# Kernel optimization log

Measured on AMD Instinct MI355X. Metric: run time of the kernel, lower is better.

Reference implementation:

```python
import jax, jax.numpy as jnp
import numpy as np

TWO_PI = 2.0 * np.pi
B, S_IN, S_OUT, K, HID = 1024, 4096, 4096, 8, 512
EPS = 1e-6


def setup_inputs() -> dict:
    key = jax.random.key(0)
    k1, k2, k3, k4, k5, k6, k7, k8 = jax.random.split(key, 8)
    x_in = jax.random.uniform(k1, (B, S_OUT), dtype=jnp.float32) * TWO_PI
    x_passive = jax.random.normal(k2, (B, S_IN), dtype=jnp.float32)
    log_density = jax.random.normal(k3, (B, 1), dtype=jnp.float32)
    # MLP params (nn.Linear default-ish init scale)
    lim1 = 1.0 / np.sqrt(S_IN)
    lim2 = 1.0 / np.sqrt(HID)
    w1 = jax.random.uniform(k4, (S_IN, HID), jnp.float32, -lim1, lim1)
    b1 = jax.random.uniform(k5, (HID,), jnp.float32, -lim1, lim1)
    w2 = jax.random.uniform(k6, (HID, S_OUT * 3 * K), jnp.float32, -lim2, lim2)
    b2 = jax.random.uniform(k7, (S_OUT * 3 * K,), jnp.float32, -lim2, lim2)
    phase_shift = jax.random.uniform(k8, (1,), jnp.float32)
    return {"x_in": x_in, "x_passive": x_passive, "log_density": log_density,
            "w1": w1, "b1": b1, "w2": w2, "b2": b2, "phase_shift": phase_shift}


def reference(x_in, x_passive, log_density, w1, b1, w2, b2, phase_shift):
    # normalise network input with global mean / (unbiased) std, as torch does
    xn = (x_passive - x_passive.mean()) / x_passive.std(ddof=1)
    # dense network: Linear -> tanh -> Linear -> tanh (final_activation=activation)
    net = jnp.tanh(jnp.tanh(xn @ w1 + b1) @ w2 + b2)            # (B, S*3K)
    net = net.reshape(-1, S_OUT, 3 * K)
    h_raw, w_raw, d_raw = net[..., :K], net[..., K:2 * K], net[..., 2 * K:]
    h_norm = jax.nn.softmax(h_raw, axis=2) * TWO_PI              # (B,S,K)
    w_norm = jax.nn.softmax(w_raw, axis=2) * TWO_PI
    d_norm = jax.nn.softplus(d_raw)
    bshape = (h_norm.shape[0], S_OUT, 1)
    x_kp = jnp.concatenate([jnp.full(bshape, -EPS, h_norm.dtype),
                            jnp.cumsum(w_norm, axis=2)], axis=2)  # (B,S,K+1)
    phi_kp = jnp.concatenate([jnp.zeros(bshape, h_norm.dtype),
                              jnp.cumsum(h_norm, axis=2)], axis=2)
    x = x_in[..., None]                                          # (B,S,1)
    # searchsorted (left) per element: count of knots strictly less than x, minus 1
    k_ind = jnp.sum(x_kp < x, axis=2, keepdims=True) - 1         # (B,S,1) int
    k_ind = jnp.clip(k_ind, 0, K - 1)
    g = lambda a, i: jnp.take_along_axis(a, i, axis=2)
    w_k = g(w_norm, k_ind)
    h_k = g(h_norm, k_ind)
    s_k = h_k / w_k
    d_k = g(d_norm, k_ind)
    d_kp1 = g(d_norm, (k_ind + 1) % K)
    x_km1 = g(x_kp, k_ind)
    phi_km1 = g(phi_kp, k_ind)
    alpha = (x - x_km1) / w_k
    a1m = alpha * (1.0 - alpha)
    denom = s_k + (d_kp1 + d_k - 2.0 * s_k) * a1m
    phi_out = (phi_km1 + h_k * (s_k * alpha ** 2 + d_k * a1m) / denom)[..., 0]
    phi_out = (phi_out + phase_shift) % TWO_PI                   # (B,S)
    grad = s_k ** 2 * (d_kp1 * alpha ** 2 + 2.0 * s_k * a1m
                       + d_k * (1.0 - alpha) ** 2) / denom ** 2  # (B,S,1)
    log_density = log_density - jnp.log(grad).sum(axis=1)        # (B,1)
    return phi_out, log_density
```

## Files before the change

### kernel.cpp

```cpp
#include <hip/hip_runtime.h>
#include <cstdint>
#include <cstddef>


typedef unsigned short u16;
typedef __bf16 bf16x8 __attribute__((ext_vector_type(8)));
typedef float f32x4 __attribute__((ext_vector_type(4)));
typedef unsigned short u16x8 __attribute__((ext_vector_type(8)));
typedef unsigned short u16x4 __attribute__((ext_vector_type(4)));
typedef unsigned short u16x2 __attribute__((ext_vector_type(2)));

#define TWOPI_F 6.28318530717958647692f

static __device__ __forceinline__ u16 f32_to_bf16(float f){
  unsigned u = __builtin_bit_cast(unsigned, f);
  return (u16)((u + 0x7fffu + ((u >> 16) & 1u)) >> 16);
}
static __device__ __forceinline__ void async16(void* lds, const void* g){
  __builtin_amdgcn_global_load_lds((const __attribute__((address_space(1))) void*)g,
                                   (__attribute__((address_space(3))) void*)lds,
                                   16, 0, 0);
}
static __device__ __forceinline__ float fast_tanh(float x){
  x = fminf(fmaxf(x, -15.f), 15.f);
  float e = __expf(2.f * x);
  return (e - 1.f) / (e + 1.f);
}
static __device__ __forceinline__ float softplus_f(float x){
  return fmaxf(x, 0.f) + __logf(1.f + __expf(-fabsf(x)));
}

__global__ void k_stats(const float* __restrict__ xp, float* __restrict__ stats){
  __shared__ float ss[4], sq[4];
  const int tid = threadIdx.x;
  const long gt = (long)blockIdx.x * 256 + tid;
  const float4* x4 = (const float4*)xp;
  float s = 0.f, q = 0.f;
  #pragma unroll
  for (int p = 0; p < 4; ++p){
    float4 v = x4[gt + (long)p * 262144];
    s += v.x + v.y + v.z + v.w;
    q += v.x*v.x + v.y*v.y + v.z*v.z + v.w*v.w;
  }
  #pragma unroll
  for (int off = 32; off; off >>= 1){
    s += __shfl_down(s, off);
    q += __shfl_down(q, off);
  }
  if ((tid & 63) == 0){ ss[tid>>6] = s; sq[tid>>6] = q; }
  __syncthreads();
  if (tid == 0){
    atomicAdd(stats,     ss[0]+ss[1]+ss[2]+ss[3]);
    atomicAdd(stats + 1, sq[0]+sq[1]+sq[2]+sq[3]);
  }
}

__global__ void k_prep(const float* __restrict__ xp, const float* __restrict__ stats,
                       u16* __restrict__ xn){
  const long t = (long)blockIdx.x * 256 + threadIdx.x;
  const float sum = stats[0], sq = stats[1];
  const float N = 4194304.f;
  const float mean = sum / N;
  const float istd = rsqrtf((sq - sum*sum/N) / (N - 1.f));
  const float4* x4 = (const float4*)xp;
  const float4 a = x4[2*t], b = x4[2*t+1];
  u16x8 o;
  o[0]=f32_to_bf16((a.x-mean)*istd); o[1]=f32_to_bf16((a.y-mean)*istd);
  o[2]=f32_to_bf16((a.z-mean)*istd); o[3]=f32_to_bf16((a.w-mean)*istd);
  o[4]=f32_to_bf16((b.x-mean)*istd); o[5]=f32_to_bf16((b.y-mean)*istd);
  o[6]=f32_to_bf16((b.z-mean)*istd); o[7]=f32_to_bf16((b.w-mean)*istd);
  ((u16x8*)xn)[t] = o;
}

__global__ __launch_bounds__(256) void k_transpose_cvt(const float* __restrict__ in,
                                                       u16* __restrict__ out,
                                                       int Kd, int Nd){
  __shared__ __align__(16) u16 tT[128*256];
  const int tid = threadIdx.x;
  const long k0 = (long)blockIdx.x * 256, n0 = (long)blockIdx.y * 128;
  const int lam = tid & 31, g = tid >> 5;
  const int c = lam * 4;
  const int sig = (lam & 7) << 2;
  #pragma unroll
  for (int pass = 0; pass < 16; ++pass){
    const int P = pass*8 + g;
    const float4 f0 = *(const float4*)&in[(k0 + 2*P    )*Nd + n0 + c];
    const float4 f1 = *(const float4*)&in[(k0 + 2*P + 1)*Nd + n0 + c];
    const int pp = 2*(P ^ sig);
    *(u16x2*)&tT[(c    )*256 + pp] = u16x2{f32_to_bf16(f0.x), f32_to_bf16(f1.x)};
    *(u16x2*)&tT[(c + 1)*256 + pp] = u16x2{f32_to_bf16(f0.y), f32_to_bf16(f1.y)};
    *(u16x2*)&tT[(c + 2)*256 + pp] = u16x2{f32_to_bf16(f0.z), f32_to_bf16(f1.z)};
    *(u16x2*)&tT[(c + 3)*256 + pp] = u16x2{f32_to_bf16(f0.w), f32_to_bf16(f1.w)};
  }
  __syncthreads();
  const int w = tid >> 6, l = tid & 63;
  const int lh = l >> 5, lk = l & 31;
  #pragma unroll
  for (int it = 0; it < 16; ++it){
    const int n = (w << 5) + (it << 1) + lh;
    const int s2 = (n >> 2) & 7;
    const u16x8 v = *(const u16x8*)&tT[n*256 + 8*(lk ^ s2)];
    *(u16x8*)&out[(n0 + n)*Kd + k0 + 8*lk] = v;
  }
}

__global__ __launch_bounds__(256, 2) void k_gemm1(
    const u16* __restrict__ xn,
    const u16* __restrict__ w1t,
    float* __restrict__ pp)
{
  __shared__ __align__(16) u16 sA[4][64*32];
  __shared__ __align__(16) u16 sB[4][64*32];
  const int tid = threadIdx.x, lane = tid & 63, w = tid >> 6;
  const int n0 = blockIdx.x << 6, m0 = blockIdx.y << 6;
  const int ks = blockIdx.z;
  const int wm = w >> 1, wn = w & 1;
  const int rA = lane >> 2, cA = (lane & 3) << 3;
  const int fr = lane & 15, fq = lane >> 4;
  const f32x4 z4 = {0.f, 0.f, 0.f, 0.f};
  f32x4 acc[2][2];
  #pragma unroll
  for (int i=0;i<2;i++){ acc[i][0] = z4; acc[i][1] = z4; }

  auto stage = [&](int kt){
    const int b = kt & 3;
    const int kofs = (ks << 11) + (kt << 5) + cA;
    async16(sA[b] + w*512, xn  + (long)(m0 + w*16 + rA)*4096 + kofs);
    async16(sB[b] + w*512, w1t + (long)(n0 + w*16 + rA)*4096 + kofs);
  };

  stage(0); stage(1);
  for (int kt = 0; kt < 64; ++kt){
    if (kt < 62){
      stage(kt + 2);
      asm volatile("s_waitcnt vmcnt(4)" ::: "memory");
    } else if (kt == 62){
      asm volatile("s_waitcnt vmcnt(2)" ::: "memory");
    } else {
      asm volatile("s_waitcnt vmcnt(0)" ::: "memory");
    }
    __builtin_amdgcn_s_barrier();
    const int b = kt & 3;
    bf16x8 af[2], bfv[2];
    #pragma unroll
    for (int i=0;i<2;i++) af[i]  = *(const bf16x8*)(sA[b] + ((wm<<5) + i*16 + fr)*32 + (fq<<3));
    #pragma unroll
    for (int j=0;j<2;j++) bfv[j] = *(const bf16x8*)(sB[b] + ((wn<<5) + j*16 + fr)*32 + (fq<<3));
    #pragma unroll
    for (int i=0;i<2;i++)
      #pragma unroll
      for (int j=0;j<2;j++)
        acc[i][j] = __builtin_amdgcn_mfma_f32_16x16x32_bf16(af[i], bfv[j], acc[i][j], 0, 0, 0);
  }
  float* po = pp + ((size_t)ks << 19);
  #pragma unroll
  for (int i=0;i<2;i++)
    #pragma unroll
    for (int j=0;j<2;j++)
      #pragma unroll
      for (int r=0;r<4;r++){
        const int row = m0 + (wm<<5) + i*16 + (fq<<2) + r;
        const int col = n0 + (wn<<5) + j*16 + fr;
        po[row*512 + col] = acc[i][j][r];
      }
}

__global__ void k_gemm1b(const float* __restrict__ pp, const float* __restrict__ b1,
                         u16* __restrict__ hb){
  const int t = blockIdx.x * 256 + threadIdx.x;
  const float4 a = ((const float4*)pp)[t];
  const float4 b = ((const float4*)pp)[131072 + t];
  const float4 bb = ((const float4*)b1)[t & 127];
  u16x4 o;
  o[0] = f32_to_bf16(fast_tanh(a.x + b.x + bb.x));
  o[1] = f32_to_bf16(fast_tanh(a.y + b.y + bb.y));
  o[2] = f32_to_bf16(fast_tanh(a.z + b.z + bb.z));
  o[3] = f32_to_bf16(fast_tanh(a.w + b.w + bb.w));
  ((u16x4*)hb)[t] = o;
}

__global__ __launch_bounds__(256, 2) void k_gemm2(
    const u16* __restrict__ hmat,
    const u16* __restrict__ w2t,
    const float* __restrict__ b2,
    const float* __restrict__ x_in,
    const float* __restrict__ phase,
    float* __restrict__ phi_out,
    float* __restrict__ part)
{
  __shared__ __align__(16) char smem[49152];

  const int tid  = threadIdx.x;
  const int lane = tid & 63;
  const int w    = tid >> 6;
  const int nt   = blockIdx.y;
  const int m0   = blockIdx.x << 8;
  const long n0  = (long)nt * 96;

  const int rA = lane >> 2, cA = (lane & 3) << 3;
  const int fr = lane & 15, fq = lane >> 4;

  const f32x4 z4 = {0.f, 0.f, 0.f, 0.f};
  f32x4 acc[4][6];
  #pragma unroll
  for (int i=0;i<4;i++)
    #pragma unroll
    for (int j=0;j<6;j++) acc[i][j] = z4;

  auto stage = [&](int kt, int b){
    const int kofs = (kt << 5) + cA;
    u16* bA = (u16*)(smem + b*24576);
    u16* bB = (u16*)(smem + b*24576 + 16384);
    #pragma unroll
    for (int cc = 0; cc < 4; ++cc){
      const int c = (w << 2) + cc;
      async16(bA + c*512, hmat + (long)(m0 + c*16 + rA)*512 + kofs);
    }
    #pragma unroll
    for (int cc = 0; cc < 2; ++cc){
      const int ch = (w << 1) + cc;
      int row = ch*16 + rA; if (row > 95) row = 95;
      async16(bB + ch*512, w2t + (n0 + row)*512 + kofs);
    }
  };

  stage(0, 0);
  #pragma unroll 2
  for (int kt = 0; kt < 16; ++kt){
    const int cur = kt & 1;
    if (kt < 15){
      stage(kt + 1, cur ^ 1);
      asm volatile("s_waitcnt vmcnt(6)" ::: "memory");
    } else {
      asm volatile("s_waitcnt vmcnt(0)" ::: "memory");
    }
    __builtin_amdgcn_s_barrier();
    const u16* bA = (const u16*)(smem + cur*24576);
    const u16* bB = (const u16*)(smem + cur*24576 + 16384);
    bf16x8 af[4], bfv[6];
    #pragma unroll
    for (int i=0;i<4;i++)
      af[i] = *(const bf16x8*)(bA + ((w<<6) + i*16 + fr)*32 + (fq<<3));
    #pragma unroll
    for (int j=0;j<6;j++)
      bfv[j] = *(const bf16x8*)(bB + (j*16 + fr)*32 + (fq<<3));
    #pragma unroll
    for (int i=0;i<4;i++)
      #pragma unroll
      for (int j=0;j<6;j++)
        acc[i][j] = __builtin_amdgcn_mfma_f32_16x16x32_bf16(af[i], bfv[j], acc[i][j], 0, 0, 0);
    __builtin_amdgcn_s_barrier();
  }

  float* sC = (float*)smem;
  const float shift = phase[0];
  float b2c[6];
  #pragma unroll
  for (int j=0;j<6;j++) b2c[j] = b2[n0 + j*16 + fr];
  float* myC = sC + w*1600;

  #pragma unroll
  for (int q = 0; q < 4; ++q){
    #pragma unroll
    for (int j=0;j<6;j++)
      #pragma unroll
      for (int r=0;r<4;r++)
        myC[((fq<<2)+r)*100 + j*16 + fr] = fast_tanh(acc[q][j][r] + b2c[j]);

    const int row = fr;
    const int g   = fq;
    const f32x4* tp4 = (const f32x4*)(myC + row*100 + g*24);
    float t[24];
    #pragma unroll
    for (int jj=0;jj<6;jj++){
      const f32x4 v = tp4[jj];
      t[4*jj] = v[0]; t[4*jj+1] = v[1]; t[4*jj+2] = v[2]; t[4*jj+3] = v[3];
    }

    const int bg = m0 + (w<<6) + (q<<4) + row;
    const int s  = (nt<<2) + g;
    const float x = x_in[(long)bg*4096 + s];

    float eh[8], ew[8];
    float sh = 0.f, sw = 0.f;
    #pragma unroll
    for (int i=0;i<8;i++){ eh[i] = __expf(t[i]);   sh += eh[i]; }
    #pragma unroll
    for (int i=0;i<8;i++){ ew[i] = __expf(t[8+i]); sw += ew[i]; }
    const float fh = TWOPI_F / sh, fw = TWOPI_F / sw;

    float cw = 0.f; int k = 0;
    #pragma unroll
    for (int i=0;i<8;i++){ cw += ew[i]*fw; k += (cw < x) ? 1 : 0; }
    if (k > 7) k = 7;

    float xkm1 = -1e-6f, ph = 0.f, wk = 0.f, hk = 0.f, dr0 = 0.f, dr1 = 0.f;
    float cw2 = 0.f, chs = 0.f;
    #pragma unroll
    for (int i=0;i<8;i++){
      const float wi = ew[i]*fw, hi = eh[i]*fh;
      if (i == k){
        wk = wi; hk = hi;
        xkm1 = (i == 0) ? -1e-6f : cw2;
        ph = chs;
        dr0 = t[16 + i];
        dr1 = t[16 + ((i+1)&7)];
      }
      cw2 += wi; chs += hi;
    }
    const float dk  = softplus_f(dr0);
    const float dk1 = softplus_f(dr1);
    const float sk  = hk / wk;
    const float alpha = (x - xkm1) / wk;
    const float a1m = alpha * (1.f - alpha);
    const float denom = sk + (dk1 + dk - 2.f*sk)*a1m;
    const float phiv = ph + hk*(sk*alpha*alpha + dk*a1m)/denom;
    float p = phiv + shift;
    if (p >= TWOPI_F) p -= TWOPI_F;
    if (p >= TWOPI_F) p -= TWOPI_F;
    phi_out[(long)bg*4096 + s] = p;

    const float om = 1.f - alpha;
    const float num = dk1*alpha*alpha + 2.f*sk*a1m + dk*om*om;
    float lg = __logf(sk*sk*num/(denom*denom));
    lg += __shfl_xor(lg, 16);
    lg += __shfl_xor(lg, 32);
    if (lane < 16) part[(long)bg*1024 + nt] = lg;
  }
}

__global__ void k_ldred(const float* __restrict__ part, const float* __restrict__ ldin,
                        float* __restrict__ ldout){
  __shared__ float ss[4];
  const int b = blockIdx.x, tid = threadIdx.x;
  const float4* p4 = (const float4*)(part + ((long)b << 10));
  const float4 v = p4[tid];
  float s = v.x + v.y + v.z + v.w;
  #pragma unroll
  for (int off = 32; off; off >>= 1) s += __shfl_down(s, off);
  if ((tid & 63) == 0) ss[tid >> 6] = s;
  __syncthreads();
  if (tid == 0) ldout[b] = ldin[b] - (ss[0]+ss[1]+ss[2]+ss[3]);
}

extern "C" void kernel_launch(void* const* d_in, const int* in_sizes, int n_in,
                              void* d_out, int out_size, void* d_ws, size_t ws_size,
                              hipStream_t stream){
  (void)in_sizes; (void)n_in; (void)out_size; (void)ws_size;
  const float* x_in  = (const float*)d_in[0];
  const float* x_pas = (const float*)d_in[1];
  const float* ldin  = (const float*)d_in[2];
  const float* w1    = (const float*)d_in[3];
  const float* b1    = (const float*)d_in[4];
  const float* w2    = (const float*)d_in[5];
  const float* b2    = (const float*)d_in[6];
  const float* phase = (const float*)d_in[7];
  float* out   = (float*)d_out;
  float* phi   = out;
  float* ldout = out + (size_t)1024*4096;

  char* ws = (char*)d_ws;
  float* stats = (float*)ws;
  u16* xn   = (u16*)(ws + 256);
  u16* w1t  = (u16*)(ws + 8388864);
  u16* hb   = (u16*)(ws + 12583168);
  u16* w2t  = (u16*)(ws + 13631744);
  float* part = (float*)(ws + 114295040);

  hipMemsetAsync(stats, 0, 8, stream);
  k_stats<<<1024, 256, 0, stream>>>(x_pas, stats);
  k_prep<<<2048, 256, 0, stream>>>(x_pas, stats, xn);
  k_transpose_cvt<<<dim3(16, 4),  256, 0, stream>>>(w1, w1t, 4096, 512);
  k_transpose_cvt<<<dim3(2, 768), 256, 0, stream>>>(w2, w2t, 512, 98304);
  k_gemm1<<<dim3(8, 16, 2), 256, 0, stream>>>(xn, w1t, part);
  k_gemm1b<<<512, 256, 0, stream>>>(part, b1, hb);
  k_gemm2<<<dim3(4, 1024), 256, 0, stream>>>(hb, w2t, b2, x_in, phase, phi, part);
  k_ldred<<<1024, 256, 0, stream>>>(part, ldin, ldout);
}
```

Measured before the change: 571.5 us.

## Single-buffer gemm2 LDS, swizzle block order, and evaluate only needed epilogue activations

```diff
diff --git a/kernel.cpp b/kernel.cpp
--- a/kernel.cpp
+++ b/kernel.cpp
@@ -21,10 +21,20 @@
                                    (__attribute__((address_space(3))) void*)lds,
                                    16, 0, 0);
 }
+static __device__ __forceinline__ float rcpf(float x){ return __builtin_amdgcn_rcpf(x); }
 static __device__ __forceinline__ float fast_tanh(float x){
   x = fminf(fmaxf(x, -15.f), 15.f);
   float e = __expf(2.f * x);
   return (e - 1.f) / (e + 1.f);
+}
+static __device__ __forceinline__ float tanh_nc(float x){
+  const float e2 = __expf(2.f * x);
+  return 1.f - 2.f * rcpf(e2 + 1.f);
+}
+static __device__ __forceinline__ float exp_tanh(float x){
+  const float e2 = __expf(2.f * x);
+  const float u  = rcpf(e2 + 1.f);
+  return __expf(1.f - 2.f * u);
 }
 static __device__ __forceinline__ float softplus_f(float x){
   return fmaxf(x, 0.f) + __logf(1.f + __expf(-fabsf(x)));
@@ -188,13 +198,18 @@
     float* __restrict__ phi_out,
     float* __restrict__ part)
 {
-  __shared__ __align__(16) char smem[49152];
+  __shared__ __align__(16) char smem[25600];
+  u16* sA = (u16*)smem;
+  u16* sB = (u16*)(smem + 16384);
+  float* sC = (float*)smem;
 
   const int tid  = threadIdx.x;
   const int lane = tid & 63;
   const int w    = tid >> 6;
-  const int nt   = blockIdx.y;
-  const int m0   = blockIdx.x << 8;
+  const int id   = blockIdx.x;
+  const int work = ((id & 7) << 9) | (id >> 3);
+  const int m0   = (work & 3) << 8;
+  const int nt   = work >> 2;
   const long n0  = (long)nt * 96;
 
   const int rA = lane >> 2, cA = (lane & 3) << 3;
@@ -207,52 +222,36 @@
     #pragma unroll
     for (int j=0;j<6;j++) acc[i][j] = z4;
 
-  auto stage = [&](int kt, int b){
+  #pragma unroll 4
+  for (int kt = 0; kt < 16; ++kt){
     const int kofs = (kt << 5) + cA;
-    u16* bA = (u16*)(smem + b*24576);
-    u16* bB = (u16*)(smem + b*24576 + 16384);
     #pragma unroll
     for (int cc = 0; cc < 4; ++cc){
       const int c = (w << 2) + cc;
-      async16(bA + c*512, hmat + (long)(m0 + c*16 + rA)*512 + kofs);
+      async16(sA + c*512, hmat + (long)(m0 + c*16 + rA)*512 + kofs);
     }
     #pragma unroll
     for (int cc = 0; cc < 2; ++cc){
       const int ch = (w << 1) + cc;
       int row = ch*16 + rA; if (row > 95) row = 95;
-      async16(bB + ch*512, w2t + (n0 + row)*512 + kofs);
-    }
-  };
-
-  stage(0, 0);
-  #pragma unroll 2
-  for (int kt = 0; kt < 16; ++kt){
-    const int cur = kt & 1;
-    if (kt < 15){
-      stage(kt + 1, cur ^ 1);
-      asm volatile("s_waitcnt vmcnt(6)" ::: "memory");
-    } else {
-      asm volatile("s_waitcnt vmcnt(0)" ::: "memory");
-    }
-    __builtin_amdgcn_s_barrier();
-    const u16* bA = (const u16*)(smem + cur*24576);
-    const u16* bB = (const u16*)(smem + cur*24576 + 16384);
+      async16(sB + ch*512, w2t + (n0 + row)*512 + kofs);
+    }
+    __syncthreads();
     bf16x8 af[4], bfv[6];
     #pragma unroll
     for (int i=0;i<4;i++)
-      af[i] = *(const bf16x8*)(bA + ((w<<6) + i*16 + fr)*32 + (fq<<3));
+      af[i] = *(const bf16x8*)(sA + ((w<<6) + i*16 + fr)*32 + (fq<<3));
     #pragma unroll
     for (int j=0;j<6;j++)
-      bfv[j] = *(const bf16x8*)(bB + (j*16 + fr)*32 + (fq<<3));
+      bfv[j] = *(const bf16x8*)(sB + (j*16 + fr)*32 + (fq<<3));
     #pragma unroll
     for (int i=0;i<4;i++)
       #pragma unroll
       for (int j=0;j<6;j++)
         acc[i][j] = __builtin_amdgcn_mfma_f32_16x16x32_bf16(af[i], bfv[j], acc[i][j], 0, 0, 0);
-    __builtin_amdgcn_s_barrier();
-  }
-
-  float* sC = (float*)smem;
+    __syncthreads();
+  }
+
   const float shift = phase[0];
   float b2c[6];
   #pragma unroll
@@ -265,15 +264,15 @@
     for (int j=0;j<6;j++)
       #pragma unroll
       for (int r=0;r<4;r++)
-        myC[((fq<<2)+r)*100 + j*16 + fr] = fast_tanh(acc[q][j][r] + b2c[j]);
+        myC[((fq<<2)+r)*100 + j*16 + fr] = acc[q][j][r] + b2c[j];
 
     const int row = fr;
     const int g   = fq;
-    const f32x4* tp4 = (const f32x4*)(myC + row*100 + g*24);
-    float t[24];
-    #pragma unroll
-    for (int jj=0;jj<6;jj++){
-      const f32x4 v = tp4[jj];
+    const float* tp = myC + row*100 + g*24;
+    float t[16];
+    #pragma unroll
+    for (int jj=0;jj<4;jj++){
+      const f32x4 v = *(const f32x4*)(tp + 4*jj);
       t[4*jj] = v[0]; t[4*jj+1] = v[1]; t[4*jj+2] = v[2]; t[4*jj+3] = v[3];
     }
 
@@ -284,37 +283,40 @@
     float eh[8], ew[8];
     float sh = 0.f, sw = 0.f;
     #pragma unroll
-    for (int i=0;i<8;i++){ eh[i] = __expf(t[i]);   sh += eh[i]; }
-    #pragma unroll
-    for (int i=0;i<8;i++){ ew[i] = __expf(t[8+i]); sw += ew[i]; }
-    const float fh = TWOPI_F / sh, fw = TWOPI_F / sw;
-
+    for (int i=0;i<8;i++){ eh[i] = exp_tanh(t[i]);   sh += eh[i]; }
+    #pragma unroll
+    for (int i=0;i<8;i++){ ew[i] = exp_tanh(t[8+i]); sw += ew[i]; }
+
+    const float xs = x * sw * (1.f / TWOPI_F);
     float cw = 0.f; int k = 0;
     #pragma unroll
-    for (int i=0;i<8;i++){ cw += ew[i]*fw; k += (cw < x) ? 1 : 0; }
+    for (int i=0;i<8;i++){ cw += ew[i]; k += (cw < xs) ? 1 : 0; }
     if (k > 7) k = 7;
 
-    float xkm1 = -1e-6f, ph = 0.f, wk = 0.f, hk = 0.f, dr0 = 0.f, dr1 = 0.f;
-    float cw2 = 0.f, chs = 0.f;
+    float wkr = 0.f, hkr = 0.f, xkr = 0.f, phr = 0.f;
+    float c2 = 0.f, h2 = 0.f;
     #pragma unroll
     for (int i=0;i<8;i++){
-      const float wi = ew[i]*fw, hi = eh[i]*fh;
-      if (i == k){
-        wk = wi; hk = hi;
-        xkm1 = (i == 0) ? -1e-6f : cw2;
-        ph = chs;
-        dr0 = t[16 + i];
-        dr1 = t[16 + ((i+1)&7)];
-      }
-      cw2 += wi; chs += hi;
-    }
-    const float dk  = softplus_f(dr0);
-    const float dk1 = softplus_f(dr1);
-    const float sk  = hk / wk;
-    const float alpha = (x - xkm1) / wk;
+      if (i == k){ wkr = ew[i]; hkr = eh[i]; xkr = c2; phr = h2; }
+      c2 += ew[i]; h2 += eh[i];
+    }
+
+    const float* dp = tp + 16;
+    const float th0 = tanh_nc(dp[k]);
+    const float th1 = tanh_nc(dp[(k + 1) & 7]);
+    const float dk  = __logf(1.f + __expf(th0));
+    const float dk1 = __logf(1.f + __expf(th1));
+
+    const float rsh = rcpf(sh);
+    const float rwk = rcpf(wkr);
+    const float alpha = (xs - xkr) * rwk;
+    const float sk = hkr * rwk * (sw * rsh);
+    const float hk = TWOPI_F * hkr * rsh;
+    const float ph = TWOPI_F * phr * rsh;
     const float a1m = alpha * (1.f - alpha);
     const float denom = sk + (dk1 + dk - 2.f*sk)*a1m;
-    const float phiv = ph + hk*(sk*alpha*alpha + dk*a1m)/denom;
+    const float rd = rcpf(denom);
+    const float phiv = ph + hk*(sk*alpha*alpha + dk*a1m)*rd;
     float p = phiv + shift;
     if (p >= TWOPI_F) p -= TWOPI_F;
     if (p >= TWOPI_F) p -= TWOPI_F;
@@ -322,7 +324,8 @@
 
     const float om = 1.f - alpha;
     const float num = dk1*alpha*alpha + 2.f*sk*a1m + dk*om*om;
-    float lg = __logf(sk*sk*num/(denom*denom));
+    const float srd = sk * rd;
+    float lg = __logf(srd*srd*num);
     lg += __shfl_xor(lg, 16);
     lg += __shfl_xor(lg, 32);
     if (lane < 16) part[(long)bg*1024 + nt] = lg;
@@ -374,6 +377,6 @@
   k_transpose_cvt<<<dim3(2, 768), 256, 0, stream>>>(w2, w2t, 512, 98304);
   k_gemm1<<<dim3(8, 16, 2), 256, 0, stream>>>(xn, w1t, part);
   k_gemm1b<<<512, 256, 0, stream>>>(part, b1, hb);
-  k_gemm2<<<dim3(4, 1024), 256, 0, stream>>>(hb, w2t, b2, x_in, phase, phi, part);
+  k_gemm2<<<dim3(4096), 256, 0, stream>>>(hb, w2t, b2, x_in, phase, phi, part);
   k_ldred<<<1024, 256, 0, stream>>>(part, ldin, ldout);
 }
```

After: 536.8 us. 6.1% less time.
